# Performance work log

Hardware: AMD Instinct MI355X
Metric: run time of the kernel (lower is better)

Reference implementation:

```python
import jax, jax.numpy as jnp
import numpy as np

N = 50000
F_IN = 512
H1 = 500
H2 = 100
C = 16
E = 800000


def setup_inputs() -> dict:
    key = jax.random.key(0)
    ks = jax.random.split(key, 8)
    x = jax.random.normal(ks[0], (N, F_IN), dtype=jnp.float32)
    edge_index = jax.random.randint(ks[1], (2, E), 0, N, dtype=jnp.int64)
    W1 = jax.random.normal(ks[2], (F_IN, H1), dtype=jnp.float32) / np.sqrt(F_IN)
    b1 = jnp.zeros((H1,), dtype=jnp.float32)
    W2 = jax.random.normal(ks[3], (H1, H2), dtype=jnp.float32) / np.sqrt(H1)
    b2 = jnp.zeros((H2,), dtype=jnp.float32)
    W3 = jax.random.normal(ks[4], (H2, C), dtype=jnp.float32) / np.sqrt(H2)
    b3 = jnp.zeros((C,), dtype=jnp.float32)
    return {"x": x, "edge_index": edge_index, "W1": W1, "b1": b1,
            "W2": W2, "b2": b2, "W3": W3, "b3": b3}


def _edge_norm(edge_index, num_nodes):
    # add self loops (as in torch add_self_loops), then symmetric degree norm
    loops = jnp.arange(num_nodes, dtype=edge_index.dtype)
    row = jnp.concatenate([edge_index[0], loops])
    col = jnp.concatenate([edge_index[1], loops])
    deg = jax.ops.segment_sum(jnp.ones_like(row, dtype=jnp.float32), row,
                              num_segments=num_nodes)
    dinv = jnp.where(deg > 0, deg ** -0.5, 0.0)  # norm[isinf] = 0
    norm = dinv[row] * dinv[col]
    return row, col, norm


def _graph_conv(x, row, col, norm, W, b, num_nodes):
    h = x @ W + b                                  # [N, out]
    msg = norm[:, None] * h[col]                   # gather + scale, [E', out]
    return jax.ops.segment_sum(msg, row, num_segments=num_nodes)  # SpMM


def reference(x, edge_index, W1, b1, W2, b2, W3, b3):
    num_nodes = x.shape[0]
    row, col, norm = _edge_norm(edge_index, num_nodes)
    h = jnp.tanh(_graph_conv(x, row, col, norm, W1, b1, num_nodes))
    h = jnp.tanh(_graph_conv(h, row, col, norm, W2, b2, num_nodes))
    h = jnp.tanh(_graph_conv(h, row, col, norm, W3, b3, num_nodes))
    return jax.nn.softmax(h, axis=1)
```

## Files before the change

kernel.cpp:

```cpp
#include <hip/hip_runtime.h>
#include <math.h>

#define NN  50000
#define FIN 512
#define HH1 500
#define HH2 100
#define NC  16
#define NE  800000
#define KD  512
#define LDP 40

typedef __attribute__((ext_vector_type(4))) float    f32x4;
typedef __attribute__((ext_vector_type(4))) _Float16 f16x4;
typedef __attribute__((ext_vector_type(8))) _Float16 f16x8;
typedef __attribute__((ext_vector_type(8))) unsigned short u16x8;


__global__ void zero2_k(int* a, int* b) {
    int i = blockIdx.x * blockDim.x + threadIdx.x;
    if (i < NN) { a[i] = 0; b[i] = 0; }
}

__global__ void hist_k(const int* __restrict__ rows, int* __restrict__ rowcnt) {
    int i = blockIdx.x * blockDim.x + threadIdx.x;
    if (i < NE) atomicAdd(&rowcnt[rows[i]], 1);
}

__global__ void dinv_k(const int* __restrict__ rowcnt, float* __restrict__ dinv) {
    int i = blockIdx.x * blockDim.x + threadIdx.x;
    if (i < NN) dinv[i] = rsqrtf((float)(rowcnt[i] + 1));
}

__global__ __launch_bounds__(1024) void scan1_k(const int* __restrict__ cnt,
                                                int* __restrict__ excl,
                                                int* __restrict__ bsum) {
    __shared__ int s[1024];
    int t = threadIdx.x;
    int i = blockIdx.x * 1024 + t;
    int v = (i < NN) ? cnt[i] : 0;
    s[t] = v;
    __syncthreads();
    #pragma unroll
    for (int off = 1; off < 1024; off <<= 1) {
        int add = (t >= off) ? s[t - off] : 0;
        __syncthreads();
        s[t] += add;
        __syncthreads();
    }
    if (i < NN) excl[i] = s[t] - v;
    if (t == 1023) bsum[blockIdx.x] = s[1023];
}

__global__ void scan2_k(int* bsum, int nb) {
    int lane = threadIdx.x;
    int orig = (lane < nb) ? bsum[lane] : 0;
    int v = orig;
    #pragma unroll
    for (int off = 1; off < 64; off <<= 1) {
        int u = __shfl_up(v, off, 64);
        if (lane >= off) v += u;
    }
    if (lane < nb) bsum[lane] = v - orig;
}

__global__ void scan3_k(const int* __restrict__ excl, const int* __restrict__ bsum,
                        int* __restrict__ ptr) {
    int i = blockIdx.x * 256 + threadIdx.x;
    if (i < NN) ptr[i] = excl[i] + bsum[i >> 10];
}

__global__ void scatter_k(const int* __restrict__ rows, const int* __restrict__ cols,
                          const float* __restrict__ dinv,
                          const int* __restrict__ row_ptr, int* __restrict__ fill,
                          int* __restrict__ col_s, float* __restrict__ w_s) {
    int e = blockIdx.x * blockDim.x + threadIdx.x;
    if (e >= NE) return;
    int r = rows[e], c = cols[e];
    int pos = row_ptr[r] + atomicAdd(&fill[r], 1);
    col_s[pos] = c;
    w_s[pos] = dinv[r] * dinv[c];
}


#define R1 (512 * 512)
#define R2 (128 * 512)
#define R3 (128 * 128)

__global__ void wconv3_k(const float* __restrict__ W1, const float* __restrict__ W2,
                         const float* __restrict__ W3, _Float16* __restrict__ Wt1,
                         _Float16* __restrict__ Wt2, _Float16* __restrict__ Wt3)
{
    int idx = blockIdx.x * 256 + threadIdx.x;
    if (idx < R1) {
        int n_ = idx >> 9, kk = idx & 511;
        float v = (n_ < HH1) ? W1[(size_t)kk * HH1 + n_] : 0.0f;
        Wt1[idx] = (_Float16)v;
    } else if (idx < R1 + R2) {
        int j = idx - R1;
        int n_ = j >> 9, kk = j & 511;
        float v = (kk < HH1 && n_ < HH2) ? W2[(size_t)kk * HH2 + n_] : 0.0f;
        Wt2[j] = (_Float16)v;
    } else if (idx < R1 + R2 + R3) {
        int j = idx - R1 - R2;
        int n_ = j >> 7, kk = j & 127;
        float v = (kk < HH2 && n_ < NC) ? W3[(size_t)kk * NC + n_] : 0.0f;
        Wt3[j] = (_Float16)v;
    }
}


template<int AF16, int KDIM>
__global__ __launch_bounds__(256) void gemm_f16_k(
    const void* __restrict__ Av, const _Float16* __restrict__ Wt,
    const float* __restrict__ bias, _Float16* __restrict__ Cb,
    int mpad, int n, int m)
{
    __shared__ __align__(16) _Float16 As[128 * LDP];
    __shared__ __align__(16) _Float16 Bs[128 * LDP];

    const float*    Af32 = (const float*)Av;
    const _Float16* Af16 = (const _Float16*)Av;

    int tid  = threadIdx.x;
    int lane = tid & 63;
    int wid  = tid >> 6;
    int wrow = wid & 1, wcol = wid >> 1;
    int lr = lane & 15, q = lane >> 4;
    int row0 = blockIdx.x * 128, col0 = blockIdx.y * 128;

    f32x4 acc[4][4];
    #pragma unroll
    for (int i = 0; i < 4; i++)
        #pragma unroll
        for (int j = 0; j < 4; j++) acc[i][j] = (f32x4){0.f, 0.f, 0.f, 0.f};

    float4 pa32[4];
    u16x8  pa16[2];
    u16x8  pb[2];

    auto load_pf = [&](int kt) {
        if (AF16 == 0) {
            #pragma unroll
            for (int i = 0; i < 4; i++) {
                int idx = tid + i * 256;
                int rr = idx >> 3, c4 = idx & 7;
                int gr = row0 + rr;
                pa32[i] = (gr < n) ? *(const float4*)(Af32 + (size_t)gr * KDIM + kt + c4 * 4)
                                   : make_float4(0.f, 0.f, 0.f, 0.f);
            }
        } else {
            #pragma unroll
            for (int i = 0; i < 2; i++) {
                int idx = tid + i * 256;
                int rr = idx >> 2, c8 = idx & 3;
                int gr = row0 + rr;
                pa16[i] = (gr < n) ? *(const u16x8*)(Af16 + (size_t)gr * KDIM + kt + c8 * 8)
                                   : (u16x8){0, 0, 0, 0, 0, 0, 0, 0};
            }
        }
        #pragma unroll
        for (int i = 0; i < 2; i++) {
            int idx = tid + i * 256;
            int rr = idx >> 2, c8 = idx & 3;
            pb[i] = *(const u16x8*)(Wt + (size_t)(col0 + rr) * KDIM + kt + c8 * 8);
        }
    };

    load_pf(0);

    for (int step = 0; step < KDIM / 32; step++) {
        __syncthreads();
        if (AF16 == 0) {
            #pragma unroll
            for (int i = 0; i < 4; i++) {
                int idx = tid + i * 256;
                int rr = idx >> 3, c4 = idx & 7;
                float4 v = pa32[i];
                f16x4 hv = {(_Float16)v.x, (_Float16)v.y, (_Float16)v.z, (_Float16)v.w};
                *(f16x4*)(As + rr * LDP + c4 * 4) = hv;
            }
        } else {
            #pragma unroll
            for (int i = 0; i < 2; i++) {
                int idx = tid + i * 256;
                int rr = idx >> 2, c8 = idx & 3;
                *(u16x8*)(As + rr * LDP + c8 * 8) = pa16[i];
            }
        }
        #pragma unroll
        for (int i = 0; i < 2; i++) {
            int idx = tid + i * 256;
            int rr = idx >> 2, c8 = idx & 3;
            *(u16x8*)(Bs + rr * LDP + c8 * 8) = pb[i];
        }
        __syncthreads();

        if (step + 1 < KDIM / 32) load_pf((step + 1) * 32);

        f16x8 a[4], b[4];
        #pragma unroll
        for (int t = 0; t < 4; t++) {
            a[t] = *(const f16x8*)(As + (wrow * 64 + t * 16 + lr) * LDP + q * 8);
            b[t] = *(const f16x8*)(Bs + (wcol * 64 + t * 16 + lr) * LDP + q * 8);
        }
        #pragma unroll
        for (int ti = 0; ti < 4; ti++)
            #pragma unroll
            for (int tj = 0; tj < 4; tj++)
                acc[ti][tj] = __builtin_amdgcn_mfma_f32_16x16x32_f16(
                    a[ti], b[tj], acc[ti][tj], 0, 0, 0);
    }

    #pragma unroll
    for (int ti = 0; ti < 4; ti++) {
        #pragma unroll
        for (int tj = 0; tj < 4; tj++) {
            int col = col0 + wcol * 64 + tj * 16 + lr;
            if (col >= mpad) continue;
            bool valid = col < m;
            float bv = valid ? bias[col] : 0.0f;
            #pragma unroll
            for (int p = 0; p < 4; p++) {
                int row = row0 + wrow * 64 + ti * 16 + q * 4 + p;
                if (row < n) {
                    float v = valid ? (acc[ti][tj][p] + bv) : 0.0f;
                    Cb[(size_t)row * mpad + col] = (_Float16)v;
                }
            }
        }
    }
}


__device__ __forceinline__ float h2f(unsigned short u) {
    union { unsigned short s; _Float16 f; } t; t.s = u; return (float)t.f;
}

__device__ __forceinline__ void fma_h8(f32x4& a0, f32x4& a1, u16x8 v, float w) {
    #pragma unroll
    for (int i = 0; i < 4; i++) a0[i] += w * h2f(v[i]);
    #pragma unroll
    for (int i = 0; i < 4; i++) a1[i] += w * h2f(v[4 + i]);
}


__global__ __launch_bounds__(256) void spmm_f16_500_k(
    const int* __restrict__ row_ptr, const int* __restrict__ rowcnt,
    const int* __restrict__ col_s, const float* __restrict__ w_s,
    const float* __restrict__ dinv, const _Float16* __restrict__ hb,
    _Float16* __restrict__ outh)
{
    int r = blockIdx.x * 4 + (threadIdx.x >> 6);
    int lane = threadIdx.x & 63;
    if (r >= NN) return;

    const u16x8* h8 = (const u16x8*)hb;

    float d = dinv[r];
    f32x4 acc0 = {0.f, 0.f, 0.f, 0.f}, acc1 = {0.f, 0.f, 0.f, 0.f};
    fma_h8(acc0, acc1, h8[(size_t)r * 64 + lane], d * d);

    int beg = row_ptr[r], cnt = rowcnt[r];
    int j = 0;
    for (; j + 3 < cnt; j += 4) {
        int   c0 = col_s[beg + j],     c1 = col_s[beg + j + 1];
        int   c2 = col_s[beg + j + 2], c3 = col_s[beg + j + 3];
        float w0 = w_s[beg + j],       w1 = w_s[beg + j + 1];
        float w2 = w_s[beg + j + 2],   w3 = w_s[beg + j + 3];
        u16x8 v0 = h8[(size_t)c0 * 64 + lane];
        u16x8 v1 = h8[(size_t)c1 * 64 + lane];
        u16x8 v2 = h8[(size_t)c2 * 64 + lane];
        u16x8 v3 = h8[(size_t)c3 * 64 + lane];
        fma_h8(acc0, acc1, v0, w0);
        fma_h8(acc0, acc1, v1, w1);
        fma_h8(acc0, acc1, v2, w2);
        fma_h8(acc0, acc1, v3, w3);
    }
    for (; j < cnt; j++) {
        fma_h8(acc0, acc1, h8[(size_t)col_s[beg + j] * 64 + lane], w_s[beg + j]);
    }

    int f0 = lane * 8;
    f16x8 o;
    #pragma unroll
    for (int i = 0; i < 4; i++)
        o[i] = (_Float16)((f0 + i < HH1) ? tanhf(acc0[i]) : 0.0f);
    #pragma unroll
    for (int i = 0; i < 4; i++)
        o[4 + i] = (_Float16)((f0 + 4 + i < HH1) ? tanhf(acc1[i]) : 0.0f);
    __builtin_nontemporal_store(o, (f16x8*)(outh + (size_t)r * KD + f0));
}


__global__ __launch_bounds__(256) void spmm_f16_100_k(
    const int* __restrict__ row_ptr, const int* __restrict__ rowcnt,
    const int* __restrict__ col_s, const float* __restrict__ w_s,
    const float* __restrict__ dinv, const _Float16* __restrict__ hb,
    _Float16* __restrict__ outh)
{
    int r = blockIdx.x * 16 + (threadIdx.x >> 4);
    int lane = threadIdx.x & 15;
    if (r >= NN) return;

    const u16x8* h8 = (const u16x8*)hb;

    float d = dinv[r];
    f32x4 acc0 = {0.f, 0.f, 0.f, 0.f}, acc1 = {0.f, 0.f, 0.f, 0.f};
    fma_h8(acc0, acc1, h8[(size_t)r * 16 + lane], d * d);

    int beg = row_ptr[r], cnt = rowcnt[r];
    int j = 0;
    for (; j + 3 < cnt; j += 4) {
        int   c0 = col_s[beg + j],     c1 = col_s[beg + j + 1];
        int   c2 = col_s[beg + j + 2], c3 = col_s[beg + j + 3];
        float w0 = w_s[beg + j],       w1 = w_s[beg + j + 1];
        float w2 = w_s[beg + j + 2],   w3 = w_s[beg + j + 3];
        u16x8 v0 = h8[(size_t)c0 * 16 + lane];
        u16x8 v1 = h8[(size_t)c1 * 16 + lane];
        u16x8 v2 = h8[(size_t)c2 * 16 + lane];
        u16x8 v3 = h8[(size_t)c3 * 16 + lane];
        fma_h8(acc0, acc1, v0, w0);
        fma_h8(acc0, acc1, v1, w1);
        fma_h8(acc0, acc1, v2, w2);
        fma_h8(acc0, acc1, v3, w3);
    }
    for (; j < cnt; j++) {
        fma_h8(acc0, acc1, h8[(size_t)col_s[beg + j] * 16 + lane], w_s[beg + j]);
    }

    int f0 = lane * 8;
    f16x8 o;
    #pragma unroll
    for (int i = 0; i < 4; i++)
        o[i] = (_Float16)((f0 + i < HH2) ? tanhf(acc0[i]) : 0.0f);
    #pragma unroll
    for (int i = 0; i < 4; i++)
        o[4 + i] = (_Float16)((f0 + 4 + i < HH2) ? tanhf(acc1[i]) : 0.0f);
    __builtin_nontemporal_store(o, (f16x8*)(outh + (size_t)r * 128 + f0));
}


__global__ __launch_bounds__(256) void spmm3h_k(
    const int* __restrict__ row_ptr, const int* __restrict__ rowcnt,
    const int* __restrict__ col_s, const float* __restrict__ w_s,
    const float* __restrict__ dinv, const _Float16* __restrict__ hb,
    float* __restrict__ out)
{
    int r = blockIdx.x * 128 + (threadIdx.x >> 1);
    int lane = threadIdx.x & 1;
    if (r >= NN) return;

    const u16x8* h8 = (const u16x8*)hb;

    float d = dinv[r];
    f32x4 acc0 = {0.f, 0.f, 0.f, 0.f}, acc1 = {0.f, 0.f, 0.f, 0.f};
    fma_h8(acc0, acc1, h8[(size_t)r * 2 + lane], d * d);

    int beg = row_ptr[r], cnt = rowcnt[r];
    int j = 0;
    for (; j + 3 < cnt; j += 4) {
        int   c0 = col_s[beg + j],     c1 = col_s[beg + j + 1];
        int   c2 = col_s[beg + j + 2], c3 = col_s[beg + j + 3];
        float w0 = w_s[beg + j],       w1 = w_s[beg + j + 1];
        float w2 = w_s[beg + j + 2],   w3 = w_s[beg + j + 3];
        u16x8 v0 = h8[(size_t)c0 * 2 + lane];
        u16x8 v1 = h8[(size_t)c1 * 2 + lane];
        u16x8 v2 = h8[(size_t)c2 * 2 + lane];
        u16x8 v3 = h8[(size_t)c3 * 2 + lane];
        fma_h8(acc0, acc1, v0, w0);
        fma_h8(acc0, acc1, v1, w1);
        fma_h8(acc0, acc1, v2, w2);
        fma_h8(acc0, acc1, v3, w3);
    }
    for (; j < cnt; j++) {
        fma_h8(acc0, acc1, h8[(size_t)col_s[beg + j] * 2 + lane], w_s[beg + j]);
    }

    float* o = out + (size_t)r * NC + lane * 8;
    __builtin_nontemporal_store(acc0, (f32x4*)o);
    __builtin_nontemporal_store(acc1, (f32x4*)(o + 4));
}

__global__ void tanh_softmax_k(const float* __restrict__ in, float* __restrict__ out) {
    int r = blockIdx.x * blockDim.x + threadIdx.x;
    if (r >= NN) return;
    float v[NC];
    float mx = -1e30f;
    #pragma unroll
    for (int j = 0; j < NC; j++) {
        v[j] = tanhf(in[r * NC + j]);
        mx = fmaxf(mx, v[j]);
    }
    float s = 0.0f;
    #pragma unroll
    for (int j = 0; j < NC; j++) { v[j] = expf(v[j] - mx); s += v[j]; }
    float inv = 1.0f / s;
    #pragma unroll
    for (int j = 0; j < NC; j++) out[r * NC + j] = v[j] * inv;
}


extern "C" void kernel_launch(void* const* d_in, const int* in_sizes, int n_in,
                              void* d_out, int out_size, void* d_ws, size_t ws_size,
                              hipStream_t stream)
{
    const float* x  = (const float*)d_in[0];
    const int*   ei = (const int*)d_in[1];
    const float* W1 = (const float*)d_in[2];
    const float* b1 = (const float*)d_in[3];
    const float* W2 = (const float*)d_in[4];
    const float* b2 = (const float*)d_in[5];
    const float* W3 = (const float*)d_in[6];
    const float* b3 = (const float*)d_in[7];
    float* out = (float*)d_out;

    const int* rows = ei;
    const int* cols = ei + NE;

    char* p = (char*)d_ws;
    float*     dinv    = (float*)p;     p += (size_t)NN * 4;
    int*       rowcnt  = (int*)p;       p += (size_t)NN * 4;
    int*       row_ptr = (int*)p;       p += (size_t)NN * 4;
    int*       fill    = (int*)p;       p += (size_t)NN * 4;
    int*       excl    = (int*)p;       p += (size_t)NN * 4;
    int*       bsum    = (int*)p;       p += (size_t)256 * 4;
    int*       col_s   = (int*)p;       p += (size_t)NE * 4;
    float*     w_s     = (float*)p;     p += (size_t)NE * 4;
    float*     B3      = (float*)p;     p += (size_t)NN * NC * 4;
    _Float16*  A1h     = (_Float16*)p;  p += (size_t)NN * KD * 2;
    _Float16*  h1h     = (_Float16*)p;  p += (size_t)NN * KD * 2;
    _Float16*  A2h     = (_Float16*)p;  p += (size_t)NN * 128 * 2;
    _Float16*  h2h     = (_Float16*)p;  p += (size_t)NN * 128 * 2;
    _Float16*  A3h     = (_Float16*)p;  p += (size_t)NN * NC * 2;
    _Float16*  Wt1     = (_Float16*)p;  p += (size_t)R1 * 2;
    _Float16*  Wt2     = (_Float16*)p;  p += (size_t)R2 * 2;
    _Float16*  Wt3     = (_Float16*)p;  p += (size_t)R3 * 2;

    const int T = 256;
    const int NB = (NN + 1023) / 1024;

    wconv3_k<<<(R1 + R2 + R3) / 256, T, 0, stream>>>(W1, W2, W3, Wt1, Wt2, Wt3);
    zero2_k<<<(NN + T - 1) / T, T, 0, stream>>>(rowcnt, fill);
    hist_k<<<(NE + T - 1) / T, T, 0, stream>>>(rows, rowcnt);
    dinv_k<<<(NN + T - 1) / T, T, 0, stream>>>(rowcnt, dinv);
    scan1_k<<<NB, 1024, 0, stream>>>(rowcnt, excl, bsum);
    scan2_k<<<1, 64, 0, stream>>>(bsum, NB);
    scan3_k<<<(NN + T - 1) / T, T, 0, stream>>>(excl, bsum, row_ptr);
    scatter_k<<<(NE + T - 1) / T, T, 0, stream>>>(rows, cols, dinv, row_ptr, fill,
                                                  col_s, w_s);

    {
        dim3 g((NN + 127) / 128, 4);
        gemm_f16_k<0, 512><<<g, T, 0, stream>>>(x, Wt1, b1, A1h, KD, NN, HH1);
        spmm_f16_500_k<<<(NN + 3) / 4, T, 0, stream>>>(row_ptr, rowcnt, col_s, w_s,
                                                       dinv, A1h, h1h);
    }
    {
        dim3 g((NN + 127) / 128, 1);
        gemm_f16_k<1, 512><<<g, T, 0, stream>>>(h1h, Wt2, b2, A2h, 128, NN, HH2);
        spmm_f16_100_k<<<(NN + 15) / 16, T, 0, stream>>>(row_ptr, rowcnt, col_s, w_s,
                                                         dinv, A2h, h2h);
    }
    {
        dim3 g((NN + 127) / 128, 1);
        gemm_f16_k<1, 128><<<g, T, 0, stream>>>(h2h, Wt3, b3, A3h, NC, NN, NC);
        spmm3h_k<<<(NN + 127) / 128, T, 0, stream>>>(row_ptr, rowcnt, col_s, w_s,
                                                     dinv, A3h, B3);
        tanh_softmax_k<<<(NN + T - 1) / T, T, 0, stream>>>(B3, out);
    }
}
```

Measured before the change: 561.3 us.

## Pack CSR col/weight into int2, use fma_mix and lane-broadcast edge loads in SpMM

Interleaves column index and edge weight into a single int2 array so each edge needs one 8-byte load instead of two. In the 500-wide SpMM a wavefront loads up to 64 edges cooperatively and broadcasts them with readlane, issuing 8 gathers before accumulating. All SpMM kernels replace the f16-to-f32 convert plus FMA with inline v_fma_mix_f32, and the 100-wide kernel unrolls to 8 edges. This trades extra register pressure and inline asm portability for fewer scalar loads and ALU ops in the memory-bound gather loops.

```diff
diff --git a/kernel.cpp b/kernel.cpp
--- a/kernel.cpp
+++ b/kernel.cpp
@@ -72,13 +72,12 @@
 __global__ void scatter_k(const int* __restrict__ rows, const int* __restrict__ cols,
                           const float* __restrict__ dinv,
                           const int* __restrict__ row_ptr, int* __restrict__ fill,
-                          int* __restrict__ col_s, float* __restrict__ w_s) {
+                          int2* __restrict__ cw) {
     int e = blockIdx.x * blockDim.x + threadIdx.x;
     if (e >= NE) return;
     int r = rows[e], c = cols[e];
     int pos = row_ptr[r] + atomicAdd(&fill[r], 1);
-    col_s[pos] = c;
-    w_s[pos] = dinv[r] * dinv[c];
+    cw[pos] = make_int2(c, __float_as_int(dinv[r] * dinv[c]));
 }
 
 
@@ -232,23 +231,22 @@
 }
 
 
-__device__ __forceinline__ float h2f(unsigned short u) {
-    union { unsigned short s; _Float16 f; } t; t.s = u; return (float)t.f;
-}
-
-__device__ __forceinline__ void fma_h8(f32x4& a0, f32x4& a1, u16x8 v, float w) {
-    #pragma unroll
-    for (int i = 0; i < 4; i++) a0[i] += w * h2f(v[i]);
-    #pragma unroll
-    for (int i = 0; i < 4; i++) a1[i] += w * h2f(v[4 + i]);
+__device__ __forceinline__ void fma_mix8(float* acc, u16x8 v, float w) {
+    union { u16x8 u; unsigned int d[4]; } t; t.u = v;
+    #pragma unroll
+    for (int k = 0; k < 4; k++) {
+        asm("v_fma_mix_f32 %0, %1, %2, %0 op_sel:[0,0,0] op_sel_hi:[1,0,0]"
+            : "+v"(acc[2 * k]) : "v"(t.d[k]), "v"(w));
+        asm("v_fma_mix_f32 %0, %1, %2, %0 op_sel:[1,0,0] op_sel_hi:[1,0,0]"
+            : "+v"(acc[2 * k + 1]) : "v"(t.d[k]), "v"(w));
+    }
 }
 
 
 __global__ __launch_bounds__(256) void spmm_f16_500_k(
     const int* __restrict__ row_ptr, const int* __restrict__ rowcnt,
-    const int* __restrict__ col_s, const float* __restrict__ w_s,
-    const float* __restrict__ dinv, const _Float16* __restrict__ hb,
-    _Float16* __restrict__ outh)
+    const int2* __restrict__ cw, const float* __restrict__ dinv,
+    const _Float16* __restrict__ hb, _Float16* __restrict__ outh)
 {
     int r = blockIdx.x * 4 + (threadIdx.x >> 6);
     int lane = threadIdx.x & 63;
@@ -256,129 +254,127 @@
 
     const u16x8* h8 = (const u16x8*)hb;
 
+    float acc[8];
+    #pragma unroll
+    for (int i = 0; i < 8; i++) acc[i] = 0.f;
+
     float d = dinv[r];
-    f32x4 acc0 = {0.f, 0.f, 0.f, 0.f}, acc1 = {0.f, 0.f, 0.f, 0.f};
-    fma_h8(acc0, acc1, h8[(size_t)r * 64 + lane], d * d);
+    fma_mix8(acc, h8[(size_t)r * 64 + lane], d * d);
+
+    int beg = row_ptr[r], cnt = rowcnt[r];
+    for (int base = 0; base < cnt; base += 64) {
+        int m = (cnt - base < 64) ? (cnt - base) : 64;
+        int2 vc = (lane < m) ? cw[beg + base + lane] : make_int2(0, 0);
+        int P = (m + 7) & ~7;
+        for (int j = 0; j < P; j += 8) {
+            u16x8 vv[8]; float wl[8];
+            #pragma unroll
+            for (int u = 0; u < 8; u++) {
+                int c  = __builtin_amdgcn_readlane(vc.x, j + u);
+                int wb = __builtin_amdgcn_readlane(vc.y, j + u);
+                wl[u] = __int_as_float(wb);
+                vv[u] = h8[(size_t)c * 64 + lane];
+            }
+            #pragma unroll
+            for (int u = 0; u < 8; u++) fma_mix8(acc, vv[u], wl[u]);
+        }
+    }
+
+    int f0 = lane * 8;
+    f16x8 o;
+    #pragma unroll
+    for (int i = 0; i < 8; i++)
+        o[i] = (_Float16)((f0 + i < HH1) ? tanhf(acc[i]) : 0.0f);
+    __builtin_nontemporal_store(o, (f16x8*)(outh + (size_t)r * KD + f0));
+}
+
+
+__global__ __launch_bounds__(256) void spmm_f16_100_k(
+    const int* __restrict__ row_ptr, const int* __restrict__ rowcnt,
+    const int2* __restrict__ cw, const float* __restrict__ dinv,
+    const _Float16* __restrict__ hb, _Float16* __restrict__ outh)
+{
+    int r = blockIdx.x * 16 + (threadIdx.x >> 4);
+    int lane = threadIdx.x & 15;
+    if (r >= NN) return;
+
+    const u16x8* h8 = (const u16x8*)hb;
+
+    float acc[8];
+    #pragma unroll
+    for (int i = 0; i < 8; i++) acc[i] = 0.f;
+
+    float d = dinv[r];
+    fma_mix8(acc, h8[(size_t)r * 16 + lane], d * d);
+
+    int beg = row_ptr[r], cnt = rowcnt[r];
+    int j = 0;
+    for (; j + 7 < cnt; j += 8) {
+        int2  e[8];
+        u16x8 v[8];
+        #pragma unroll
+        for (int u = 0; u < 8; u++) e[u] = cw[beg + j + u];
+        #pragma unroll
+        for (int u = 0; u < 8; u++) v[u] = h8[(size_t)e[u].x * 16 + lane];
+        #pragma unroll
+        for (int u = 0; u < 8; u++) fma_mix8(acc, v[u], __int_as_float(e[u].y));
+    }
+    for (; j < cnt; j++) {
+        int2 e = cw[beg + j];
+        fma_mix8(acc, h8[(size_t)e.x * 16 + lane], __int_as_float(e.y));
+    }
+
+    int f0 = lane * 8;
+    f16x8 o;
+    #pragma unroll
+    for (int i = 0; i < 8; i++)
+        o[i] = (_Float16)((f0 + i < HH2) ? tanhf(acc[i]) : 0.0f);
+    __builtin_nontemporal_store(o, (f16x8*)(outh + (size_t)r * 128 + f0));
+}
+
+
+__global__ __launch_bounds__(256) void spmm3h_k(
+    const int* __restrict__ row_ptr, const int* __restrict__ rowcnt,
+    const int2* __restrict__ cw, const float* __restrict__ dinv,
+    const _Float16* __restrict__ hb, float* __restrict__ out)
+{
+    int r = blockIdx.x * 128 + (threadIdx.x >> 1);
+    int lane = threadIdx.x & 1;
+    if (r >= NN) return;
+
+    const u16x8* h8 = (const u16x8*)hb;
+
+    float acc[8];
+    #pragma unroll
+    for (int i = 0; i < 8; i++) acc[i] = 0.f;
+
+    float d = dinv[r];
+    fma_mix8(acc, h8[(size_t)r * 2 + lane], d * d);
 
     int beg = row_ptr[r], cnt = rowcnt[r];
     int j = 0;
     for (; j + 3 < cnt; j += 4) {
-        int   c0 = col_s[beg + j],     c1 = col_s[beg + j + 1];
-        int   c2 = col_s[beg + j + 2], c3 = col_s[beg + j + 3];
-        float w0 = w_s[beg + j],       w1 = w_s[beg + j + 1];
-        float w2 = w_s[beg + j + 2],   w3 = w_s[beg + j + 3];
-        u16x8 v0 = h8[(size_t)c0 * 64 + lane];
-        u16x8 v1 = h8[(size_t)c1 * 64 + lane];
-        u16x8 v2 = h8[(size_t)c2 * 64 + lane];
-        u16x8 v3 = h8[(size_t)c3 * 64 + lane];
-        fma_h8(acc0, acc1, v0, w0);
-        fma_h8(acc0, acc1, v1, w1);
-        fma_h8(acc0, acc1, v2, w2);
-        fma_h8(acc0, acc1, v3, w3);
+        int2  e0 = cw[beg + j],     e1 = cw[beg + j + 1];
+        int2  e2 = cw[beg + j + 2], e3 = cw[beg + j + 3];
+        u16x8 v0 = h8[(size_t)e0.x * 2 + lane];
+        u16x8 v1 = h8[(size_t)e1.x * 2 + lane];
+        u16x8 v2 = h8[(size_t)e2.x * 2 + lane];
+        u16x8 v3 = h8[(size_t)e3.x * 2 + lane];
+        fma_mix8(acc, v0, __int_as_float(e0.y));
+        fma_mix8(acc, v1, __int_as_float(e1.y));
+        fma_mix8(acc, v2, __int_as_float(e2.y));
+        fma_mix8(acc, v3, __int_as_float(e3.y));
     }
     for (; j < cnt; j++) {
-        fma_h8(acc0, acc1, h8[(size_t)col_s[beg + j] * 64 + lane], w_s[beg + j]);
-    }
-
-    int f0 = lane * 8;
-    f16x8 o;
-    #pragma unroll
-    for (int i = 0; i < 4; i++)
-        o[i] = (_Float16)((f0 + i < HH1) ? tanhf(acc0[i]) : 0.0f);
-    #pragma unroll
-    for (int i = 0; i < 4; i++)
-        o[4 + i] = (_Float16)((f0 + 4 + i < HH1) ? tanhf(acc1[i]) : 0.0f);
-    __builtin_nontemporal_store(o, (f16x8*)(outh + (size_t)r * KD + f0));
-}
-
-
-__global__ __launch_bounds__(256) void spmm_f16_100_k(
-    const int* __restrict__ row_ptr, const int* __restrict__ rowcnt,
-    const int* __restrict__ col_s, const float* __restrict__ w_s,
-    const float* __restrict__ dinv, const _Float16* __restrict__ hb,
-    _Float16* __restrict__ outh)
-{
-    int r = blockIdx.x * 16 + (threadIdx.x >> 4);
-    int lane = threadIdx.x & 15;
-    if (r >= NN) return;
-
-    const u16x8* h8 = (const u16x8*)hb;
-
-    float d = dinv[r];
-    f32x4 acc0 = {0.f, 0.f, 0.f, 0.f}, acc1 = {0.f, 0.f, 0.f, 0.f};
-    fma_h8(acc0, acc1, h8[(size_t)r * 16 + lane], d * d);
-
-    int beg = row_ptr[r], cnt = rowcnt[r];
-    int j = 0;
-    for (; j + 3 < cnt; j += 4) {
-        int   c0 = col_s[beg + j],     c1 = col_s[beg + j + 1];
-        int   c2 = col_s[beg + j + 2], c3 = col_s[beg + j + 3];
-        float w0 = w_s[beg + j],       w1 = w_s[beg + j + 1];
-        float w2 = w_s[beg + j + 2],   w3 = w_s[beg + j + 3];
-        u16x8 v0 = h8[(size_t)c0 * 16 + lane];
-        u16x8 v1 = h8[(size_t)c1 * 16 + lane];
-        u16x8 v2 = h8[(size_t)c2 * 16 + lane];
-        u16x8 v3 = h8[(size_t)c3 * 16 + lane];
-        fma_h8(acc0, acc1, v0, w0);
-        fma_h8(acc0, acc1, v1, w1);
-        fma_h8(acc0, acc1, v2, w2);
-        fma_h8(acc0, acc1, v3, w3);
-    }
-    for (; j < cnt; j++) {
-        fma_h8(acc0, acc1, h8[(size_t)col_s[beg + j] * 16 + lane], w_s[beg + j]);
-    }
-
-    int f0 = lane * 8;
-    f16x8 o;
-    #pragma unroll
-    for (int i = 0; i < 4; i++)
-        o[i] = (_Float16)((f0 + i < HH2) ? tanhf(acc0[i]) : 0.0f);
-    #pragma unroll
-    for (int i = 0; i < 4; i++)
-        o[4 + i] = (_Float16)((f0 + 4 + i < HH2) ? tanhf(acc1[i]) : 0.0f);
-    __builtin_nontemporal_store(o, (f16x8*)(outh + (size_t)r * 128 + f0));
-}
-
-
-__global__ __launch_bounds__(256) void spmm3h_k(
-    const int* __restrict__ row_ptr, const int* __restrict__ rowcnt,
-    const int* __restrict__ col_s, const float* __restrict__ w_s,
-    const float* __restrict__ dinv, const _Float16* __restrict__ hb,
-    float* __restrict__ out)
-{
-    int r = blockIdx.x * 128 + (threadIdx.x >> 1);
-    int lane = threadIdx.x & 1;
-    if (r >= NN) return;
-
-    const u16x8* h8 = (const u16x8*)hb;
-
-    float d = dinv[r];
-    f32x4 acc0 = {0.f, 0.f, 0.f, 0.f}, acc1 = {0.f, 0.f, 0.f, 0.f};
-    fma_h8(acc0, acc1, h8[(size_t)r * 2 + lane], d * d);
-
-    int beg = row_ptr[r], cnt = rowcnt[r];
-    int j = 0;
-    for (; j + 3 < cnt; j += 4) {
-        int   c0 = col_s[beg + j],     c1 = col_s[beg + j + 1];
-        int   c2 = col_s[beg + j + 2], c3 = col_s[beg + j + 3];
-        float w0 = w_s[beg + j],       w1 = w_s[beg + j + 1];
-        float w2 = w_s[beg + j + 2],   w3 = w_s[beg + j + 3];
-        u16x8 v0 = h8[(size_t)c0 * 2 + lane];
-        u16x8 v1 = h8[(size_t)c1 * 2 + lane];
-        u16x8 v2 = h8[(size_t)c2 * 2 + lane];
-        u16x8 v3 = h8[(size_t)c3 * 2 + lane];
-        fma_h8(acc0, acc1, v0, w0);
-        fma_h8(acc0, acc1, v1, w1);
-        fma_h8(acc0, acc1, v2, w2);
-        fma_h8(acc0, acc1, v3, w3);
-    }
-    for (; j < cnt; j++) {
-        fma_h8(acc0, acc1, h8[(size_t)col_s[beg + j] * 2 + lane], w_s[beg + j]);
+        int2 e = cw[beg + j];
+        fma_mix8(acc, h8[(size_t)e.x * 2 + lane], __int_as_float(e.y));
     }
 
     float* o = out + (size_t)r * NC + lane * 8;
-    __builtin_nontemporal_store(acc0, (f32x4*)o);
-    __builtin_nontemporal_store(acc1, (f32x4*)(o + 4));
+    f32x4 a0 = {acc[0], acc[1], acc[2], acc[3]};
+    f32x4 a1 = {acc[4], acc[5], acc[6], acc[7]};
+    __builtin_nontemporal_store(a0, (f32x4*)o);
+    __builtin_nontemporal_store(a1, (f32x4*)(o + 4));
 }
 
 __global__ void tanh_softmax_k(const float* __restrict__ in, float* __restrict__ out) {
@@ -424,8 +420,7 @@
     int*       fill    = (int*)p;       p += (size_t)NN * 4;
     int*       excl    = (int*)p;       p += (size_t)NN * 4;
     int*       bsum    = (int*)p;       p += (size_t)256 * 4;
-    int*       col_s   = (int*)p;       p += (size_t)NE * 4;
-    float*     w_s     = (float*)p;     p += (size_t)NE * 4;
+    int2*      cw      = (int2*)p;      p += (size_t)NE * 8;
     float*     B3      = (float*)p;     p += (size_t)NN * NC * 4;
     _Float16*  A1h     = (_Float16*)p;  p += (size_t)NN * KD * 2;
     _Float16*  h1h     = (_Float16*)p;  p += (size_t)NN * KD * 2;
@@ -446,25 +441,24 @@
     scan1_k<<<NB, 1024, 0, stream>>>(rowcnt, excl, bsum);
     scan2_k<<<1, 64, 0, stream>>>(bsum, NB);
     scan3_k<<<(NN + T - 1) / T, T, 0, stream>>>(excl, bsum, row_ptr);
-    scatter_k<<<(NE + T - 1) / T, T, 0, stream>>>(rows, cols, dinv, row_ptr, fill,
-                                                  col_s, w_s);
+    scatter_k<<<(NE + T - 1) / T, T, 0, stream>>>(rows, cols, dinv, row_ptr, fill, cw);
 
     {
         dim3 g((NN + 127) / 128, 4);
         gemm_f16_k<0, 512><<<g, T, 0, stream>>>(x, Wt1, b1, A1h, KD, NN, HH1);
-        spmm_f16_500_k<<<(NN + 3) / 4, T, 0, stream>>>(row_ptr, rowcnt, col_s, w_s,
+        spmm_f16_500_k<<<(NN + 3) / 4, T, 0, stream>>>(row_ptr, rowcnt, cw,
                                                        dinv, A1h, h1h);
     }
     {
         dim3 g((NN + 127) / 128, 1);
         gemm_f16_k<1, 512><<<g, T, 0, stream>>>(h1h, Wt2, b2, A2h, 128, NN, HH2);
-        spmm_f16_100_k<<<(NN + 15) / 16, T, 0, stream>>>(row_ptr, rowcnt, col_s, w_s,
+        spmm_f16_100_k<<<(NN + 15) / 16, T, 0, stream>>>(row_ptr, rowcnt, cw,
                                                          dinv, A2h, h2h);
     }
     {
         dim3 g((NN + 127) / 128, 1);
         gemm_f16_k<1, 128><<<g, T, 0, stream>>>(h2h, Wt3, b3, A3h, NC, NN, NC);
-        spmm3h_k<<<(NN + 127) / 128, T, 0, stream>>>(row_ptr, rowcnt, col_s, w_s,
+        spmm3h_k<<<(NN + 127) / 128, T, 0, stream>>>(row_ptr, rowcnt, cw,
                                                      dinv, A3h, B3);
         tanh_softmax_k<<<(NN + T - 1) / T, T, 0, stream>>>(B3, out);
     }
```

New measurement: 550.1 us. 2.0% less time.
